# Optimization experiments

Hardware: AMD Instinct MI355X
Metric: run time of the kernel (lower is better)

## Reference

```python
import jax, jax.numpy as jnp
import numpy as np

# LIF constants (match init_kwargs)
T, B, N = 512, 64, 4096
V_TH0 = 1.0
V_RESET = 0.0
TAU = 20.0
DT = 1.0
ETA = 0.1
MIN_TH = 0.5
MAX_TH = 2.0


def setup_inputs() -> dict:
    key = jax.random.key(0)
    input_data = jax.random.normal(key, (T, B, N), dtype=jnp.float32)
    return {"input_data": input_data}


def reference(input_data):
    """LIF recurrence over timesteps, deterministic (no noise), heaviside spikes,
    adaptive threshold clamped to [MIN_TH, MAX_TH]. Returns spikes [T,B,N]."""
    decay = jnp.float32(DT / TAU)
    v0 = jnp.zeros((B, N), dtype=jnp.float32)           # membrane potential
    th0 = jnp.full((B, N), V_TH0, dtype=jnp.float32)    # adaptive threshold

    def step(carry, I_t):
        V, Vth = carry
        V = V + decay * (I_t - V)                       # leaky integration
        spikes = (V >= Vth).astype(jnp.float32)         # heaviside fire
        V = V * (1.0 - spikes) + V_RESET * spikes       # reset where spiked
        Vth = jnp.clip(Vth + ETA * spikes, MIN_TH, MAX_TH)  # threshold adaptation
        return (V, Vth), spikes

    _, out_spikes = jax.lax.scan(step, (v0, th0), input_data)
    return out_spikes
```

## Files before the change

kernel.cpp:

```cpp
#include <hip/hip_runtime.h>


typedef float f32x4 __attribute__((ext_vector_type(4)));

namespace {
constexpr int kT   = 512;
constexpr int kB   = 64;
constexpr int kN   = 4096;
constexpr int kBN  = kB * kN;
constexpr int kBN4 = kBN / 4;
constexpr float kDecay = 0.05f;
constexpr float kEta   = 0.1f;
constexpr float kMinTh = 0.5f;
constexpr float kMaxTh = 2.0f;
}

__global__ __launch_bounds__(256) void lif_kernel(const f32x4* __restrict__ in,
                                                  f32x4* __restrict__ out) {
#pragma clang fp contract(off)
  const int col = blockIdx.x * blockDim.x + threadIdx.x;

  f32x4 V  = {0.0f, 0.0f, 0.0f, 0.0f};
  f32x4 Th = {1.0f, 1.0f, 1.0f, 1.0f};

  const f32x4* ip = in + col;
  f32x4* op = out + col;

#pragma unroll 8
  for (int t = 0; t < kT; ++t) {
    const f32x4 I = __builtin_nontemporal_load(ip);
    f32x4 S;

#define LIF_STEP(c)                                              \
    {                                                            \
      float d = I.c - V.c;                                       \
      float p = kDecay * d;                                      \
      float v = V.c + p;                                         \
      float s = (v >= Th.c) ? 1.0f : 0.0f;                       \
      V.c = (v >= Th.c) ? 0.0f : v;                              \
      S.c = s;                                                   \
      Th.c = fminf(fmaxf(Th.c + kEta * s, kMinTh), kMaxTh);      \
    }

    LIF_STEP(x)
    LIF_STEP(y)
    LIF_STEP(z)
    LIF_STEP(w)
#undef LIF_STEP

    __builtin_nontemporal_store(S, op);
    ip += kBN4;
    op += kBN4;
  }
}

extern "C" void kernel_launch(void* const* d_in, const int* in_sizes, int n_in,
                              void* d_out, int out_size, void* d_ws, size_t ws_size,
                              hipStream_t stream) {
  const f32x4* in = reinterpret_cast<const f32x4*>(d_in[0]);
  f32x4* out = reinterpret_cast<f32x4*>(d_out);

  const int threads = 256;
  const int blocks = kBN4 / threads;
  lif_kernel<<<dim3(blocks), dim3(threads), 0, stream>>>(in, out);
}
```

Before: 828.2 us.

## Use float2 per thread and batch 16 timestep loads per group

Halves the work per thread so twice as many threads run, and prefetches 16 timesteps of input into registers before computing and storing them in batches. The goal is more memory-level parallelism and occupancy for a latency-bound streaming recurrence. Nontemporal load/store hints are dropped, and register use grows with the buffers.

```diff
diff --git a/kernel.cpp b/kernel.cpp
--- a/kernel.cpp
+++ b/kernel.cpp
@@ -1,66 +1,77 @@
 #include <hip/hip_runtime.h>
 
 
-typedef float f32x4 __attribute__((ext_vector_type(4)));
+typedef float f32x2 __attribute__((ext_vector_type(2)));
 
 namespace {
 constexpr int kT   = 512;
 constexpr int kB   = 64;
 constexpr int kN   = 4096;
 constexpr int kBN  = kB * kN;
-constexpr int kBN4 = kBN / 4;
+constexpr int kBN2 = kBN / 2;
+constexpr int kU   = 16;
 constexpr float kDecay = 0.05f;
 constexpr float kEta   = 0.1f;
 constexpr float kMinTh = 0.5f;
 constexpr float kMaxTh = 2.0f;
 }
 
-__global__ __launch_bounds__(256) void lif_kernel(const f32x4* __restrict__ in,
-                                                  f32x4* __restrict__ out) {
+__global__ __launch_bounds__(256) void lif_kernel(const f32x2* __restrict__ in,
+                                                  f32x2* __restrict__ out) {
 #pragma clang fp contract(off)
   const int col = blockIdx.x * blockDim.x + threadIdx.x;
 
-  f32x4 V  = {0.0f, 0.0f, 0.0f, 0.0f};
-  f32x4 Th = {1.0f, 1.0f, 1.0f, 1.0f};
+  f32x2 V  = {0.0f, 0.0f};
+  f32x2 Th = {1.0f, 1.0f};
 
-  const f32x4* ip = in + col;
-  f32x4* op = out + col;
+  const f32x2* ip = in + col;
+  f32x2* op = out + col;
 
-#pragma unroll 8
-  for (int t = 0; t < kT; ++t) {
-    const f32x4 I = __builtin_nontemporal_load(ip);
-    f32x4 S;
-
-#define LIF_STEP(c)                                              \
-    {                                                            \
-      float d = I.c - V.c;                                       \
-      float p = kDecay * d;                                      \
-      float v = V.c + p;                                         \
-      float s = (v >= Th.c) ? 1.0f : 0.0f;                       \
-      V.c = (v >= Th.c) ? 0.0f : v;                              \
-      S.c = s;                                                   \
-      Th.c = fminf(fmaxf(Th.c + kEta * s, kMinTh), kMaxTh);      \
+  for (int g = 0; g < kT / kU; ++g) {
+    f32x2 Ibuf[kU];
+#pragma unroll
+    for (int u = 0; u < kU; ++u) {
+      Ibuf[u] = ip[u * kBN2];
     }
 
-    LIF_STEP(x)
-    LIF_STEP(y)
-    LIF_STEP(z)
-    LIF_STEP(w)
+    f32x2 Sbuf[kU];
+#pragma unroll
+    for (int u = 0; u < kU; ++u) {
+      const f32x2 I = Ibuf[u];
+      f32x2 S;
+#define LIF_STEP(c)                                              \
+      {                                                          \
+        float d = I.c - V.c;                                     \
+        float p = kDecay * d;                                    \
+        float v = V.c + p;                                       \
+        float s = (v >= Th.c) ? 1.0f : 0.0f;                     \
+        V.c = (v >= Th.c) ? 0.0f : v;                            \
+        S.c = s;                                                 \
+        Th.c = fminf(fmaxf(Th.c + kEta * s, kMinTh), kMaxTh);    \
+      }
+      LIF_STEP(x)
+      LIF_STEP(y)
 #undef LIF_STEP
+      Sbuf[u] = S;
+    }
 
-    __builtin_nontemporal_store(S, op);
-    ip += kBN4;
-    op += kBN4;
+#pragma unroll
+    for (int u = 0; u < kU; ++u) {
+      op[u * kBN2] = Sbuf[u];
+    }
+
+    ip += kU * kBN2;
+    op += kU * kBN2;
   }
 }
 
 extern "C" void kernel_launch(void* const* d_in, const int* in_sizes, int n_in,
                               void* d_out, int out_size, void* d_ws, size_t ws_size,
                               hipStream_t stream) {
-  const f32x4* in = reinterpret_cast<const f32x4*>(d_in[0]);
-  f32x4* out = reinterpret_cast<f32x4*>(d_out);
+  const f32x2* in = reinterpret_cast<const f32x2*>(d_in[0]);
+  f32x2* out = reinterpret_cast<f32x2*>(d_out);
 
   const int threads = 256;
-  const int blocks = kBN4 / threads;
+  const int blocks = kBN2 / threads;
   lif_kernel<<<dim3(blocks), dim3(threads), 0, stream>>>(in, out);
 }
```

After: 833.5 us. Within noise of the previous version (+0.6%).
